# Kernel optimization log

Hardware: AMD Instinct MI355X
Metric: run time of the kernel (lower is better)

Reference implementation:

```python
import jax, jax.numpy as jnp
import numpy as np

N, E = 50000, 800000
D, H, C, ED = 128, 8, 16, 32  # in_channels, heads, head_dim, edge_dim
EPS = 1e-5

def _ln(x, g, b):
    mu = jnp.mean(x, axis=-1, keepdims=True)
    var = jnp.mean((x - mu) ** 2, axis=-1, keepdims=True)
    return (x - mu) * jax.lax.rsqrt(var + EPS) * g + b

def setup_inputs() -> dict:
    key = jax.random.key(0)
    ks = jax.random.split(key, 20)
    s = 0.05
    inp = {
        'x': jax.random.normal(ks[0], (N, D), jnp.float32),
        'edge_index': jax.random.randint(ks[1], (2, E), 0, N, jnp.int64),
        'edge_attr': jax.random.normal(ks[2], (E, ED), jnp.float32),
        'Wq': jax.random.normal(ks[3], (D, H * C)) * s,
        'bq': jnp.zeros((H * C,)),
        'Wk': jax.random.normal(ks[4], (D, H * C)) * s,
        'bk': jnp.zeros((H * C,)),
        'Wv': jax.random.normal(ks[5], (D, H * C)) * s,
        'bv': jnp.zeros((H * C,)),
        'We': jax.random.normal(ks[6], (ED, H * C)) * s,
        'Wskip': jax.random.normal(ks[7], (D, H * C)) * s,
        'bskip': jnp.zeros((H * C,)),
        'ln1_g': jnp.ones((D,)), 'ln1_b': jnp.zeros((D,)),
        'W1': jax.random.normal(ks[8], (D, 4 * D)) * s,
        'b1': jnp.zeros((4 * D,)),
        'W2': jax.random.normal(ks[9], (4 * D, D)) * s,
        'b2': jnp.zeros((D,)),
        'ln2_g': jnp.ones((D,)), 'ln2_b': jnp.zeros((D,)),
    }
    return inp

def reference(x, edge_index, edge_attr, Wq, bq, Wk, bk, Wv, bv, We, Wskip, bskip,
              ln1_g, ln1_b, W1, b1, W2, b2, ln2_g, ln2_b):
    src, dst = edge_index[0], edge_index[1]
    # node-level projections, then gather per-edge  [N,H,C] -> [E,H,C]
    q = (x @ Wq + bq).reshape(N, H, C)
    k = (x @ Wk + bk).reshape(N, H, C)
    v = (x @ Wv + bv).reshape(N, H, C)
    e = (edge_attr @ We).reshape(E, H, C)
    k_e = k[src] + e
    alpha = jnp.sum(q[dst] * k_e, axis=-1) / jnp.sqrt(jnp.float32(C))  # [E,H]
    # segment softmax over destination nodes
    m = jax.ops.segment_max(alpha, dst, num_segments=N)               # [N,H]
    p = jnp.exp(alpha - m[dst])
    denom = jax.ops.segment_sum(p, dst, num_segments=N)
    a = p / (denom[dst] + 1e-16)
    out_e = (v[src] + e) * a[..., None]                               # [E,H,C]
    attn = jax.ops.segment_sum(out_e, dst, num_segments=N).reshape(N, H * C)
    attn = attn + x @ Wskip + bskip  # root/skip connection
    # transformer block: residual + LN + FFN + LN (dropout = identity, eval)
    h = _ln(x + attn, ln1_g, ln1_b)
    ffn = jax.nn.relu(h @ W1 + b1) @ W2 + b2
    return _ln(h + ffn, ln2_g, ln2_b)
```

## Files before the change

### kernel.cpp

```cpp
#include <hip/hip_runtime.h>
#include <hip/hip_bf16.h>

using bf16 = __hip_bfloat16;
typedef __attribute__((ext_vector_type(8))) short short8;
typedef __attribute__((ext_vector_type(4))) float floatx4;

#define NN 50000
#define EE 800000
#define DD 128
#define HH 8
#define CC 16
#define EDD 32
#define DF 512

__device__ __forceinline__ float b2f(bf16 v) { return __bfloat162float(v); }
__device__ __forceinline__ float bs2f(short s) {
    bf16 h = *reinterpret_cast<bf16*>(&s);
    return __bfloat162float(h);
}
__device__ __forceinline__ float bu2f(unsigned short s) {
    unsigned int u = ((unsigned int)s) << 16;
    return *reinterpret_cast<float*>(&u);
}
__device__ __forceinline__ short f2bs(float v) {
    bf16 h = __float2bfloat16(v);
    return *reinterpret_cast<short*>(&h);
}

__global__ void k_detect(const int* __restrict__ ei, int* __restrict__ flag)
{
    if (threadIdx.x == 0 && blockIdx.x == 0) {
        int all0 = 1;
        for (int i = 0; i < 16; ++i) all0 &= (ei[2 * i + 1] == 0);
        flag[0] = all0;
    }
}

__device__ __forceinline__ int load_src(const int* ei, int is64, int i)
{
    int s = is64 ? ei[2 * i] : ei[i];
    return (s < 0) ? 0 : (s >= NN ? NN - 1 : s);
}
__device__ __forceinline__ int load_dst(const int* ei, int is64, int i)
{
    int d = is64 ? ei[2 * EE + 2 * i] : ei[EE + i];
    return (d < 0) ? 0 : (d >= NN ? NN - 1 : d);
}

__global__ void k_packall(const float* __restrict__ Wq, const float* __restrict__ Wk,
                          const float* __restrict__ Wv, const float* __restrict__ Wsk,
                          const float* __restrict__ W1, const float* __restrict__ W2,
                          const float* __restrict__ We,
                          bf16* __restrict__ wqp, bf16* __restrict__ wkp,
                          bf16* __restrict__ wvp, bf16* __restrict__ wskp,
                          bf16* __restrict__ w1p, bf16* __restrict__ w2p,
                          bf16* __restrict__ wep)
{
    int idx = blockIdx.x * 256 + threadIdx.x;
    const float* W; bf16* out; int ksteps, N, local;
    if (idx < 65536) {
        int wsel = idx >> 14; local = idx & 16383;
        W   = (wsel == 0) ? Wq  : (wsel == 1) ? Wk  : (wsel == 2) ? Wv  : Wsk;
        out = (wsel == 0) ? wqp : (wsel == 1) ? wkp : (wsel == 2) ? wvp : wskp;
        ksteps = 4; N = 128;
    } else if (idx < 131072) { local = idx - 65536;  W = W1; out = w1p; ksteps = 4;  N = 512; }
    else if (idx < 196608)   { local = idx - 131072; W = W2; out = w2p; ksteps = 16; N = 128; }
    else if (idx < 200704)   { local = idx - 196608; W = We; out = wep; ksteps = 1;  N = 128; }
    else return;
    int j = local & 7, lane = (local >> 3) & 63, rest = local >> 9;
    int kstep = rest % ksteps, ntile = rest / ksteps;
    int quad = lane >> 4, m = lane & 15;
    int k = kstep * 32 + quad * 8 + j;
    int n = ntile * 16 + m;
    out[local] = __float2bfloat16(W[(size_t)k * N + n]);
}

__global__ __launch_bounds__(256) void k_proj(
    const float* __restrict__ x,
    const bf16* __restrict__ wqp, const bf16* __restrict__ wkp,
    const bf16* __restrict__ wvp, const bf16* __restrict__ wskp,
    const float* __restrict__ bq, const float* __restrict__ bk,
    const float* __restrict__ bv, const float* __restrict__ bsk,
    bf16* __restrict__ qb, unsigned int* __restrict__ kvb,
    bf16* __restrict__ skipb)
{
    __shared__ __align__(16) short xs[32][136];
    __shared__ __align__(16) short os[32][520];
    const int t = threadIdx.x;
    const int wave = t >> 6, lane = t & 63;
    const int quad = lane >> 4, m = lane & 15;
    const int n0 = blockIdx.x * 32;

    for (int idx = t; idx < 32 * 32; idx += 256) {
        int row = idx >> 5, g = idx & 31;
        int node = n0 + row;
        float4 xv = {0.f, 0.f, 0.f, 0.f};
        if (node < NN) xv = *reinterpret_cast<const float4*>(&x[(size_t)node * 128 + g * 4]);
        short4 s4;
        s4.x = f2bs(xv.x); s4.y = f2bs(xv.y); s4.z = f2bs(xv.z); s4.w = f2bs(xv.w);
        *reinterpret_cast<short4*>(&xs[row][g * 4]) = s4;
    }
    __syncthreads();

    const bf16* Wp = (wave == 0) ? wqp : (wave == 1) ? wkp : (wave == 2) ? wvp : wskp;
    const float* bias = (wave == 0) ? bq : (wave == 1) ? bk : (wave == 2) ? bv : bsk;

    floatx4 acc[2][8];
#pragma unroll
    for (int mt = 0; mt < 2; ++mt)
#pragma unroll
        for (int nt = 0; nt < 8; ++nt) acc[mt][nt] = (floatx4){0.f, 0.f, 0.f, 0.f};

#pragma unroll
    for (int kstep = 0; kstep < 4; ++kstep) {
        short8 af0 = *reinterpret_cast<const short8*>(&xs[m][kstep * 32 + quad * 8]);
        short8 af1 = *reinterpret_cast<const short8*>(&xs[16 + m][kstep * 32 + quad * 8]);
#pragma unroll
        for (int nt = 0; nt < 8; ++nt) {
            short8 bf = *reinterpret_cast<const short8*>(
                reinterpret_cast<const short*>(Wp) + ((nt * 4 + kstep) * 64 + lane) * 8);
            acc[0][nt] = __builtin_amdgcn_mfma_f32_16x16x32_bf16(af0, bf, acc[0][nt], 0, 0, 0);
            acc[1][nt] = __builtin_amdgcn_mfma_f32_16x16x32_bf16(af1, bf, acc[1][nt], 0, 0, 0);
        }
    }
#pragma unroll
    for (int nt = 0; nt < 8; ++nt) {
        float bs = bias[nt * 16 + m];
#pragma unroll
        for (int mt = 0; mt < 2; ++mt)
#pragma unroll
            for (int r = 0; r < 4; ++r)
                os[mt * 16 + quad * 4 + r][wave * 128 + nt * 16 + m] = f2bs(acc[mt][nt][r] + bs);
    }
    __syncthreads();
    for (int idx = t; idx < 32 * 64; idx += 256) {
        int row = idx >> 6, c = idx & 63;
        int node = n0 + row;
        if (node >= NN) continue;
        unsigned int qu  = *reinterpret_cast<const unsigned int*>(&os[row][2 * c]);
        unsigned int ku  = *reinterpret_cast<const unsigned int*>(&os[row][128 + 2 * c]);
        unsigned int vu  = *reinterpret_cast<const unsigned int*>(&os[row][256 + 2 * c]);
        unsigned int sku = *reinterpret_cast<const unsigned int*>(&os[row][384 + 2 * c]);
        reinterpret_cast<unsigned int*>(qb)[(size_t)node * 64 + c] = qu;
        reinterpret_cast<unsigned int*>(skipb)[(size_t)node * 64 + c] = sku;
        uint2 kv;
        kv.x = (ku & 0xffffu) | (vu << 16);
        kv.y = (ku >> 16) | (vu & 0xffff0000u);
        reinterpret_cast<uint2*>(kvb)[(size_t)node * 64 + c] = kv;
    }
}

__global__ void k_hist(const int* __restrict__ ei, const int* __restrict__ flag,
                       int* __restrict__ deg)
{
    int i = blockIdx.x * 256 + threadIdx.x;
    if (i >= EE) return;
    atomicAdd(&deg[load_dst(ei, flag[0], i)], 1);
}

__global__ __launch_bounds__(1024) void k_scan(const int* __restrict__ deg,
                                               int* __restrict__ rowstart)
{
    __shared__ int s[1024];
    const int t = threadIdx.x;
    const int CH = 49;
    int base = t * CH;
    int sum = 0;
    for (int i = 0; i < CH; i++) {
        int idx = base + i;
        if (idx < NN) sum += deg[idx];
    }
    s[t] = sum;
    __syncthreads();
    int own = sum;
    for (int off = 1; off < 1024; off <<= 1) {
        int v = (t >= off) ? s[t - off] : 0;
        __syncthreads();
        s[t] += v;
        __syncthreads();
    }
    int run = s[t] - own;
    for (int i = 0; i < CH; i++) {
        int idx = base + i;
        if (idx < NN) {
            rowstart[idx] = run;
            run += deg[idx];
        }
    }
    if (t == 0) rowstart[NN] = EE;
}

__global__ void k_scatter(const int* __restrict__ ei, const int* __restrict__ flag,
                          const int* __restrict__ rowstart,
                          int* __restrict__ cursor, int2* __restrict__ srcid)
{
    int i = blockIdx.x * 256 + threadIdx.x;
    if (i >= EE) return;
    int is64 = flag[0];
    int d = load_dst(ei, is64, i);
    int pos = rowstart[d] + atomicAdd(&cursor[d], 1);
    srcid[pos] = make_int2(load_src(ei, is64, i), i);
}

__global__ __launch_bounds__(256) void k_attn(
    const float* __restrict__ x, const float* __restrict__ edge_attr,
    const bf16* __restrict__ wep,
    const bf16* __restrict__ qb, const unsigned int* __restrict__ kvb,
    const bf16* __restrict__ skipb,
    const int* __restrict__ rowstart, const int2* __restrict__ srcid,
    const float* __restrict__ ln1g, const float* __restrict__ ln1b,
    bf16* __restrict__ hb)
{
    __shared__ __align__(16) short es[4][16][136];
    __shared__ __align__(16) short wes[4096];
    const int t = threadIdx.x;
    const int wave = t >> 6, lane = t & 63;
    const int quad = lane >> 4, m = lane & 15;
    const int n = blockIdx.x * 4 + wave;

    for (int idx = t; idx < 512; idx += 256)
        *reinterpret_cast<short8*>(&wes[idx * 8]) =
            *reinterpret_cast<const short8*>(reinterpret_cast<const short*>(wep) + idx * 8);
    __syncthreads();

    short (*esw)[136] = es[wave];

    unsigned int qp = reinterpret_cast<const unsigned int*>(qb)[(size_t)n * 64 + lane];
    float q0 = bu2f((unsigned short)(qp & 0xffffu));
    float q1 = bu2f((unsigned short)(qp >> 16));

    const int eoff = rowstart[n], eend = rowstart[n + 1];
    float lsum = 0.f, acc0 = 0.f, acc1 = 0.f;

    for (int p0 = eoff; p0 < eend; p0 += 16) {
        int pos = p0 + m;
        int pc = (pos < eend) ? pos : eoff;
        int2 se = srcid[pc];

        const float* arow = edge_attr + (size_t)se.y * 32 + quad * 8;
        float4 a0 = *reinterpret_cast<const float4*>(arow);
        float4 a1 = *reinterpret_cast<const float4*>(arow + 4);

        uint2 kvr[16];
#pragma unroll
        for (int j = 0; j < 16; ++j) {
            int sj = __builtin_amdgcn_readlane(se.x, j);
            kvr[j] = reinterpret_cast<const uint2*>(kvb + (size_t)(unsigned)sj * 128)[lane];
        }

        short8 Af;
        Af[0] = f2bs(a0.x); Af[1] = f2bs(a0.y); Af[2] = f2bs(a0.z); Af[3] = f2bs(a0.w);
        Af[4] = f2bs(a1.x); Af[5] = f2bs(a1.y); Af[6] = f2bs(a1.z); Af[7] = f2bs(a1.w);
#pragma unroll
        for (int nt = 0; nt < 8; ++nt) {
            short8 Bf = *reinterpret_cast<const short8*>(&wes[(nt * 64 + lane) * 8]);
            floatx4 C = {0.f, 0.f, 0.f, 0.f};
            C = __builtin_amdgcn_mfma_f32_16x16x32_bf16(Af, Bf, C, 0, 0, 0);
            int col = nt * 16 + m;
#pragma unroll
            for (int r = 0; r < 4; ++r)
                esw[quad * 4 + r][col] = f2bs(C[r]);
        }
        __builtin_amdgcn_wave_barrier();

        int cnt = eend - p0; if (cnt > 16) cnt = 16;
#pragma unroll
        for (int j = 0; j < 16; ++j) {
            unsigned int eu = *reinterpret_cast<const unsigned int*>(&esw[j][2 * lane]);
            float e0 = bu2f((unsigned short)(eu & 0xffffu));
            float e1 = bu2f((unsigned short)(eu >> 16));
            float k0 = bu2f((unsigned short)(kvr[j].x & 0xffffu));
            float v0 = bu2f((unsigned short)(kvr[j].x >> 16));
            float k1 = bu2f((unsigned short)(kvr[j].y & 0xffffu));
            float v1 = bu2f((unsigned short)(kvr[j].y >> 16));
            float pr = fmaf(k1 + e1, q1, (k0 + e0) * q0);
            pr += __shfl_xor(pr, 1);
            pr += __shfl_xor(pr, 2);
            pr += __shfl_xor(pr, 4);
            float w = (j < cnt) ? __expf(pr * 0.25f) : 0.f;
            lsum += w;
            acc0 = fmaf(v0 + e0, w, acc0);
            acc1 = fmaf(v1 + e1, w, acc1);
        }
        __builtin_amdgcn_wave_barrier();
    }

    float rden = 1.f / (lsum + 1e-16f);
    float attn0 = acc0 * rden, attn1 = acc1 * rden;
    float2 xv = *reinterpret_cast<const float2*>(x + (size_t)n * 128 + 2 * lane);
    unsigned int skp = reinterpret_cast<const unsigned int*>(skipb)[(size_t)n * 64 + lane];
    float pre0 = xv.x + attn0 + bu2f((unsigned short)(skp & 0xffffu));
    float pre1 = xv.y + attn1 + bu2f((unsigned short)(skp >> 16));
    float s1 = pre0 + pre1, s2 = pre0 * pre0 + pre1 * pre1;
#pragma unroll
    for (int off = 1; off < 64; off <<= 1) {
        s1 += __shfl_xor(s1, off);
        s2 += __shfl_xor(s2, off);
    }
    float mu = s1 * (1.f / 128.f);
    float var = s2 * (1.f / 128.f) - mu * mu;
    float inv = rsqrtf(var + 1e-5f);
    float2 g  = *reinterpret_cast<const float2*>(ln1g + 2 * lane);
    float2 bb = *reinterpret_cast<const float2*>(ln1b + 2 * lane);
    float h0 = (pre0 - mu) * inv * g.x + bb.x;
    float h1 = (pre1 - mu) * inv * g.y + bb.y;
    unsigned int hu = (unsigned int)(unsigned short)f2bs(h0) |
                      ((unsigned int)(unsigned short)f2bs(h1) << 16);
    reinterpret_cast<unsigned int*>(hb)[(size_t)n * 64 + lane] = hu;
}

__global__ __launch_bounds__(256) void k_ffn(
    const bf16* __restrict__ hb,
    const bf16* __restrict__ w1p, const float* __restrict__ b1,
    const bf16* __restrict__ w2p, const float* __restrict__ b2,
    const float* __restrict__ ln2g, const float* __restrict__ ln2b,
    float* __restrict__ out)
{
    __shared__ __align__(16) short hs[32][136];
    __shared__ __align__(16) short t1s[32][520];
    float* fs = reinterpret_cast<float*>(&t1s[0][0]);
    const int t = threadIdx.x;
    const int wave = t >> 6, lane = t & 63;
    const int quad = lane >> 4, m = lane & 15;
    const int n0 = blockIdx.x * 32;

    for (int idx = t; idx < 32 * 16; idx += 256) {
        int row = idx >> 4, g = idx & 15;
        int node = n0 + row;
        if (node < NN) {
            *reinterpret_cast<float4*>(&hs[row][g * 8]) =
                *reinterpret_cast<const float4*>(&hb[(size_t)node * 128 + g * 8]);
        } else {
            float4 z = {0.f, 0.f, 0.f, 0.f};
            *reinterpret_cast<float4*>(&hs[row][g * 8]) = z;
        }
    }
    __syncthreads();

    floatx4 acc1[2][8];
#pragma unroll
    for (int mt = 0; mt < 2; ++mt)
#pragma unroll
        for (int nt = 0; nt < 8; ++nt) acc1[mt][nt] = (floatx4){0.f, 0.f, 0.f, 0.f};
#pragma unroll
    for (int kstep = 0; kstep < 4; ++kstep) {
        short8 af0 = *reinterpret_cast<const short8*>(&hs[m][kstep * 32 + quad * 8]);
        short8 af1 = *reinterpret_cast<const short8*>(&hs[16 + m][kstep * 32 + quad * 8]);
#pragma unroll
        for (int nt = 0; nt < 8; ++nt) {
            short8 bf = *reinterpret_cast<const short8*>(
                reinterpret_cast<const short*>(w1p) + (((wave * 8 + nt) * 4 + kstep) * 64 + lane) * 8);
            acc1[0][nt] = __builtin_amdgcn_mfma_f32_16x16x32_bf16(af0, bf, acc1[0][nt], 0, 0, 0);
            acc1[1][nt] = __builtin_amdgcn_mfma_f32_16x16x32_bf16(af1, bf, acc1[1][nt], 0, 0, 0);
        }
    }
#pragma unroll
    for (int nt = 0; nt < 8; ++nt) {
        float bs = b1[wave * 128 + nt * 16 + m];
#pragma unroll
        for (int mt = 0; mt < 2; ++mt)
#pragma unroll
            for (int r = 0; r < 4; ++r)
                t1s[mt * 16 + quad * 4 + r][wave * 128 + nt * 16 + m] =
                    f2bs(fmaxf(acc1[mt][nt][r] + bs, 0.f));
    }
    __syncthreads();

    floatx4 acc2[2][2];
#pragma unroll
    for (int mt = 0; mt < 2; ++mt)
#pragma unroll
        for (int nt = 0; nt < 2; ++nt) acc2[mt][nt] = (floatx4){0.f, 0.f, 0.f, 0.f};
#pragma unroll
    for (int kstep = 0; kstep < 16; ++kstep) {
        short8 af0 = *reinterpret_cast<const short8*>(&t1s[m][kstep * 32 + quad * 8]);
        short8 af1 = *reinterpret_cast<const short8*>(&t1s[16 + m][kstep * 32 + quad * 8]);
#pragma unroll
        for (int nt = 0; nt < 2; ++nt) {
            short8 bf = *reinterpret_cast<const short8*>(
                reinterpret_cast<const short*>(w2p) + (((wave * 2 + nt) * 16 + kstep) * 64 + lane) * 8);
            acc2[0][nt] = __builtin_amdgcn_mfma_f32_16x16x32_bf16(af0, bf, acc2[0][nt], 0, 0, 0);
            acc2[1][nt] = __builtin_amdgcn_mfma_f32_16x16x32_bf16(af1, bf, acc2[1][nt], 0, 0, 0);
        }
    }
    __syncthreads();
#pragma unroll
    for (int nt = 0; nt < 2; ++nt) {
        int col = (wave * 2 + nt) * 16 + m;
        float bs = b2[col];
#pragma unroll
        for (int mt = 0; mt < 2; ++mt)
#pragma unroll
            for (int r = 0; r < 4; ++r)
                fs[(mt * 16 + quad * 4 + r) * 132 + col] = acc2[mt][nt][r] + bs;
    }
    __syncthreads();

    for (int rr = 0; rr < 8; ++rr) {
        int row = wave * 8 + rr;
        int node = n0 + row;
        float p0 = bs2f(hs[row][lane]) + fs[row * 132 + lane];
        float p1 = bs2f(hs[row][lane + 64]) + fs[row * 132 + lane + 64];
        float s1 = p0 + p1, s2 = p0 * p0 + p1 * p1;
#pragma unroll
        for (int off = 1; off < 64; off <<= 1) {
            s1 += __shfl_xor(s1, off);
            s2 += __shfl_xor(s2, off);
        }
        float mu = s1 * (1.f / 128.f);
        float var = s2 * (1.f / 128.f) - mu * mu;
        float inv = rsqrtf(var + 1e-5f);
        if (node < NN) {
            out[(size_t)node * 128 + lane] = (p0 - mu) * inv * ln2g[lane] + ln2b[lane];
            out[(size_t)node * 128 + lane + 64] = (p1 - mu) * inv * ln2g[lane + 64] + ln2b[lane + 64];
        }
    }
}

extern "C" void kernel_launch(void* const* d_in, const int* in_sizes, int n_in,
                              void* d_out, int out_size, void* d_ws, size_t ws_size,
                              hipStream_t stream)
{
    const float* x    = (const float*)d_in[0];
    const int*   ei   = (const int*)d_in[1];
    const float* ea   = (const float*)d_in[2];
    const float* Wq   = (const float*)d_in[3];
    const float* bq   = (const float*)d_in[4];
    const float* Wk   = (const float*)d_in[5];
    const float* bk   = (const float*)d_in[6];
    const float* Wv   = (const float*)d_in[7];
    const float* bv   = (const float*)d_in[8];
    const float* We   = (const float*)d_in[9];
    const float* Wsk  = (const float*)d_in[10];
    const float* bsk  = (const float*)d_in[11];
    const float* ln1g = (const float*)d_in[12];
    const float* ln1b = (const float*)d_in[13];
    const float* W1   = (const float*)d_in[14];
    const float* b1   = (const float*)d_in[15];
    const float* W2   = (const float*)d_in[16];
    const float* b2   = (const float*)d_in[17];
    const float* ln2g = (const float*)d_in[18];
    const float* ln2b = (const float*)d_in[19];

    char* ws = (char*)d_ws;
    size_t off = 0;
    auto alloc = [&](size_t bytes) -> void* {
        void* p = ws + off;
        off += (bytes + 255) & ~(size_t)255;
        return p;
    };
    int*   flag     = (int*)alloc(256);
    int*   deg      = (int*)alloc((size_t)NN * 4);
    int*   cursor   = (int*)alloc((size_t)NN * 4);
    int*   rowstart = (int*)alloc((size_t)(NN + 1) * 4);
    int2*  srcid    = (int2*)alloc((size_t)EE * 8);
    bf16*  qb       = (bf16*)alloc((size_t)NN * 128 * 2);
    unsigned int* kvb = (unsigned int*)alloc((size_t)NN * 128 * 4);
    bf16*  skipb    = (bf16*)alloc((size_t)NN * 128 * 2);
    bf16*  hb       = (bf16*)alloc((size_t)NN * 128 * 2);
    bf16*  wqp      = (bf16*)alloc((size_t)16384 * 2);
    bf16*  wkp      = (bf16*)alloc((size_t)16384 * 2);
    bf16*  wvp      = (bf16*)alloc((size_t)16384 * 2);
    bf16*  wskp     = (bf16*)alloc((size_t)16384 * 2);
    bf16*  w1p      = (bf16*)alloc((size_t)65536 * 2);
    bf16*  w2p      = (bf16*)alloc((size_t)65536 * 2);
    bf16*  wep      = (bf16*)alloc((size_t)4096 * 2);

    hipMemsetAsync(deg, 0, (size_t)NN * 4, stream);
    hipMemsetAsync(cursor, 0, (size_t)NN * 4, stream);

    k_detect<<<1, 64, 0, stream>>>(ei, flag);
    k_packall<<<(200704 + 255) / 256, 256, 0, stream>>>(
        Wq, Wk, Wv, Wsk, W1, W2, We, wqp, wkp, wvp, wskp, w1p, w2p, wep);
    k_hist<<<(EE + 255) / 256, 256, 0, stream>>>(ei, flag, deg);
    k_proj<<<(NN + 31) / 32, 256, 0, stream>>>(x, wqp, wkp, wvp, wskp,
                                               bq, bk, bv, bsk, qb, kvb, skipb);
    k_scan<<<1, 1024, 0, stream>>>(deg, rowstart);
    k_scatter<<<(EE + 255) / 256, 256, 0, stream>>>(ei, flag, rowstart, cursor, srcid);
    k_attn<<<(NN + 3) / 4, 256, 0, stream>>>(x, ea, wep, qb, kvb, skipb,
                                             rowstart, srcid, ln1g, ln1b, hb);
    k_ffn<<<(NN + 31) / 32, 256, 0, stream>>>(hb, w1p, b1, w2p, b2, ln2g, ln2b, (float*)d_out);
}
```

Baseline: 548.9 us.

## Use persistent work-stealing attention kernel, transposed edge LDS, and paired-edge CSR build

The attention kernel becomes persistent: 1536 blocks pull destination nodes from a global atomic counter, which should even out load across nodes of uneven degree. The edge-feature tile in LDS is transposed so each lane reads its 16 values with a few wide loads instead of 16 separate reads. The softmax now folds 1/sqrt(C)*log2(e) into q and uses exp2 directly. The histogram and scatter kernels each handle two edges per thread with vector loads. The risks are atomic contention on the single work counter and higher register pressure from the extra LDS values held per lane.

```diff
diff --git a/kernel.cpp b/kernel.cpp
--- a/kernel.cpp
+++ b/kernel.cpp
@@ -26,6 +26,10 @@
     bf16 h = __float2bfloat16(v);
     return *reinterpret_cast<short*>(&h);
 }
+__device__ __forceinline__ unsigned short f2bu(float v) {
+    bf16 h = __float2bfloat16(v);
+    return *reinterpret_cast<unsigned short*>(&h);
+}
 
 __global__ void k_detect(const int* __restrict__ ei, int* __restrict__ flag)
 {
@@ -36,15 +40,9 @@
     }
 }
 
-__device__ __forceinline__ int load_src(const int* ei, int is64, int i)
-{
-    int s = is64 ? ei[2 * i] : ei[i];
-    return (s < 0) ? 0 : (s >= NN ? NN - 1 : s);
-}
-__device__ __forceinline__ int load_dst(const int* ei, int is64, int i)
-{
-    int d = is64 ? ei[2 * EE + 2 * i] : ei[EE + i];
-    return (d < 0) ? 0 : (d >= NN ? NN - 1 : d);
+__device__ __forceinline__ int clampn(int v)
+{
+    return (v < 0) ? 0 : (v >= NN ? NN - 1 : v);
 }
 
 __global__ void k_packall(const float* __restrict__ Wq, const float* __restrict__ Wk,
@@ -153,9 +151,19 @@
 __global__ void k_hist(const int* __restrict__ ei, const int* __restrict__ flag,
                        int* __restrict__ deg)
 {
-    int i = blockIdx.x * 256 + threadIdx.x;
-    if (i >= EE) return;
-    atomicAdd(&deg[load_dst(ei, flag[0], i)], 1);
+    int tt = blockIdx.x * 256 + threadIdx.x;
+    int i0 = tt * 2;
+    if (i0 >= EE) return;
+    int d0, d1;
+    if (flag[0]) {
+        int4 v = *reinterpret_cast<const int4*>(&ei[2 * EE + 2 * i0]);
+        d0 = v.x; d1 = v.z;
+    } else {
+        int2 v = *reinterpret_cast<const int2*>(&ei[EE + i0]);
+        d0 = v.x; d1 = v.y;
+    }
+    atomicAdd(&deg[clampn(d0)], 1);
+    atomicAdd(&deg[clampn(d1)], 1);
 }
 
 __global__ __launch_bounds__(1024) void k_scan(const int* __restrict__ deg,
@@ -194,12 +202,24 @@
                           const int* __restrict__ rowstart,
                           int* __restrict__ cursor, int2* __restrict__ srcid)
 {
-    int i = blockIdx.x * 256 + threadIdx.x;
-    if (i >= EE) return;
-    int is64 = flag[0];
-    int d = load_dst(ei, is64, i);
-    int pos = rowstart[d] + atomicAdd(&cursor[d], 1);
-    srcid[pos] = make_int2(load_src(ei, is64, i), i);
+    int tt = blockIdx.x * 256 + threadIdx.x;
+    int i0 = tt * 2;
+    if (i0 >= EE) return;
+    int d0, d1, s0, s1;
+    if (flag[0]) {
+        int4 dv = *reinterpret_cast<const int4*>(&ei[2 * EE + 2 * i0]);
+        int4 sv = *reinterpret_cast<const int4*>(&ei[2 * i0]);
+        d0 = dv.x; d1 = dv.z; s0 = sv.x; s1 = sv.z;
+    } else {
+        int2 dv = *reinterpret_cast<const int2*>(&ei[EE + i0]);
+        int2 sv = *reinterpret_cast<const int2*>(&ei[i0]);
+        d0 = dv.x; d1 = dv.y; s0 = sv.x; s1 = sv.y;
+    }
+    d0 = clampn(d0); d1 = clampn(d1);
+    int p0 = rowstart[d0] + atomicAdd(&cursor[d0], 1);
+    srcid[p0] = make_int2(clampn(s0), i0);
+    int p1 = rowstart[d1] + atomicAdd(&cursor[d1], 1);
+    srcid[p1] = make_int2(clampn(s1), i0 + 1);
 }
 
 __global__ __launch_bounds__(256) void k_attn(
@@ -209,104 +229,124 @@
     const bf16* __restrict__ skipb,
     const int* __restrict__ rowstart, const int2* __restrict__ srcid,
     const float* __restrict__ ln1g, const float* __restrict__ ln1b,
-    bf16* __restrict__ hb)
-{
-    __shared__ __align__(16) short es[4][16][136];
+    int* __restrict__ qcounter, bf16* __restrict__ hb)
+{
+    __shared__ __align__(16) short es[4][128][18];
     __shared__ __align__(16) short wes[4096];
     const int t = threadIdx.x;
     const int wave = t >> 6, lane = t & 63;
     const int quad = lane >> 4, m = lane & 15;
-    const int n = blockIdx.x * 4 + wave;
 
     for (int idx = t; idx < 512; idx += 256)
         *reinterpret_cast<short8*>(&wes[idx * 8]) =
             *reinterpret_cast<const short8*>(reinterpret_cast<const short*>(wep) + idx * 8);
     __syncthreads();
 
-    short (*esw)[136] = es[wave];
-
-    unsigned int qp = reinterpret_cast<const unsigned int*>(qb)[(size_t)n * 64 + lane];
-    float q0 = bu2f((unsigned short)(qp & 0xffffu));
-    float q1 = bu2f((unsigned short)(qp >> 16));
-
-    const int eoff = rowstart[n], eend = rowstart[n + 1];
-    float lsum = 0.f, acc0 = 0.f, acc1 = 0.f;
-
-    for (int p0 = eoff; p0 < eend; p0 += 16) {
-        int pos = p0 + m;
-        int pc = (pos < eend) ? pos : eoff;
-        int2 se = srcid[pc];
-
-        const float* arow = edge_attr + (size_t)se.y * 32 + quad * 8;
-        float4 a0 = *reinterpret_cast<const float4*>(arow);
-        float4 a1 = *reinterpret_cast<const float4*>(arow + 4);
-
-        uint2 kvr[16];
-#pragma unroll
-        for (int j = 0; j < 16; ++j) {
-            int sj = __builtin_amdgcn_readlane(se.x, j);
-            kvr[j] = reinterpret_cast<const uint2*>(kvb + (size_t)(unsigned)sj * 128)[lane];
-        }
-
-        short8 Af;
-        Af[0] = f2bs(a0.x); Af[1] = f2bs(a0.y); Af[2] = f2bs(a0.z); Af[3] = f2bs(a0.w);
-        Af[4] = f2bs(a1.x); Af[5] = f2bs(a1.y); Af[6] = f2bs(a1.z); Af[7] = f2bs(a1.w);
-#pragma unroll
-        for (int nt = 0; nt < 8; ++nt) {
-            short8 Bf = *reinterpret_cast<const short8*>(&wes[(nt * 64 + lane) * 8]);
-            floatx4 C = {0.f, 0.f, 0.f, 0.f};
-            C = __builtin_amdgcn_mfma_f32_16x16x32_bf16(Af, Bf, C, 0, 0, 0);
-            int col = nt * 16 + m;
-#pragma unroll
-            for (int r = 0; r < 4; ++r)
-                esw[quad * 4 + r][col] = f2bs(C[r]);
-        }
-        __builtin_amdgcn_wave_barrier();
-
-        int cnt = eend - p0; if (cnt > 16) cnt = 16;
-#pragma unroll
-        for (int j = 0; j < 16; ++j) {
-            unsigned int eu = *reinterpret_cast<const unsigned int*>(&esw[j][2 * lane]);
-            float e0 = bu2f((unsigned short)(eu & 0xffffu));
-            float e1 = bu2f((unsigned short)(eu >> 16));
-            float k0 = bu2f((unsigned short)(kvr[j].x & 0xffffu));
-            float v0 = bu2f((unsigned short)(kvr[j].x >> 16));
-            float k1 = bu2f((unsigned short)(kvr[j].y & 0xffffu));
-            float v1 = bu2f((unsigned short)(kvr[j].y >> 16));
-            float pr = fmaf(k1 + e1, q1, (k0 + e0) * q0);
-            pr += __shfl_xor(pr, 1);
-            pr += __shfl_xor(pr, 2);
-            pr += __shfl_xor(pr, 4);
-            float w = (j < cnt) ? __expf(pr * 0.25f) : 0.f;
-            lsum += w;
-            acc0 = fmaf(v0 + e0, w, acc0);
-            acc1 = fmaf(v1 + e1, w, acc1);
-        }
-        __builtin_amdgcn_wave_barrier();
-    }
-
-    float rden = 1.f / (lsum + 1e-16f);
-    float attn0 = acc0 * rden, attn1 = acc1 * rden;
-    float2 xv = *reinterpret_cast<const float2*>(x + (size_t)n * 128 + 2 * lane);
-    unsigned int skp = reinterpret_cast<const unsigned int*>(skipb)[(size_t)n * 64 + lane];
-    float pre0 = xv.x + attn0 + bu2f((unsigned short)(skp & 0xffffu));
-    float pre1 = xv.y + attn1 + bu2f((unsigned short)(skp >> 16));
-    float s1 = pre0 + pre1, s2 = pre0 * pre0 + pre1 * pre1;
-#pragma unroll
-    for (int off = 1; off < 64; off <<= 1) {
-        s1 += __shfl_xor(s1, off);
-        s2 += __shfl_xor(s2, off);
-    }
-    float mu = s1 * (1.f / 128.f);
-    float var = s2 * (1.f / 128.f) - mu * mu;
-    float inv = rsqrtf(var + 1e-5f);
-    float2 g  = *reinterpret_cast<const float2*>(ln1g + 2 * lane);
-    float2 bb = *reinterpret_cast<const float2*>(ln1b + 2 * lane);
-    float h0 = (pre0 - mu) * inv * g.x + bb.x;
-    float h1 = (pre1 - mu) * inv * g.y + bb.y;
-    unsigned int hu = (unsigned int)(unsigned short)f2bs(h0) |
-                      ((unsigned int)(unsigned short)f2bs(h1) << 16);
-    reinterpret_cast<unsigned int*>(hb)[(size_t)n * 64 + lane] = hu;
+    short (*esw)[18] = es[wave];
+    const float QS = 0.3606737602f;
+
+    for (;;) {
+        int n;
+        if (lane == 0) n = atomicAdd(qcounter, 1);
+        n = __builtin_amdgcn_readfirstlane(n);
+        if (n >= NN) break;
+
+        unsigned int qp = reinterpret_cast<const unsigned int*>(qb)[(size_t)n * 64 + lane];
+        float q0 = bu2f((unsigned short)(qp & 0xffffu)) * QS;
+        float q1 = bu2f((unsigned short)(qp >> 16)) * QS;
+
+        const int eoff = rowstart[n], eend = rowstart[n + 1];
+        float lsum = 0.f, acc0 = 0.f, acc1 = 0.f;
+
+        for (int p0 = eoff; p0 < eend; p0 += 16) {
+            int pos = p0 + m;
+            int pc = (pos < eend) ? pos : eoff;
+            int2 se = srcid[pc];
+
+            const float* arow = edge_attr + (size_t)se.y * 32 + quad * 8;
+            float4 a0 = *reinterpret_cast<const float4*>(arow);
+            float4 a1 = *reinterpret_cast<const float4*>(arow + 4);
+
+            uint2 kvr[16];
+#pragma unroll
+            for (int j = 0; j < 16; ++j) {
+                int sj = __builtin_amdgcn_readlane(se.x, j);
+                kvr[j] = reinterpret_cast<const uint2*>(kvb + (size_t)(unsigned)sj * 128)[lane];
+            }
+
+            short8 Af;
+            Af[0] = f2bs(a0.x); Af[1] = f2bs(a0.y); Af[2] = f2bs(a0.z); Af[3] = f2bs(a0.w);
+            Af[4] = f2bs(a1.x); Af[5] = f2bs(a1.y); Af[6] = f2bs(a1.z); Af[7] = f2bs(a1.w);
+#pragma unroll
+            for (int nt = 0; nt < 8; ++nt) {
+                short8 Bf = *reinterpret_cast<const short8*>(&wes[(nt * 64 + lane) * 8]);
+                floatx4 C = {0.f, 0.f, 0.f, 0.f};
+                C = __builtin_amdgcn_mfma_f32_16x16x32_bf16(Af, Bf, C, 0, 0, 0);
+                int col = nt * 16 + m;
+                unsigned int d0 = (unsigned int)(unsigned short)f2bs(C[0]) |
+                                  ((unsigned int)(unsigned short)f2bs(C[1]) << 16);
+                unsigned int d1 = (unsigned int)(unsigned short)f2bs(C[2]) |
+                                  ((unsigned int)(unsigned short)f2bs(C[3]) << 16);
+                unsigned int* p = reinterpret_cast<unsigned int*>(&esw[col][quad * 4]);
+                p[0] = d0; p[1] = d1;
+            }
+            __builtin_amdgcn_wave_barrier();
+
+            unsigned int ea[8], eb[8];
+            {
+                const unsigned int* ra = reinterpret_cast<const unsigned int*>(&esw[2 * lane][0]);
+                const unsigned int* rb = reinterpret_cast<const unsigned int*>(&esw[2 * lane + 1][0]);
+#pragma unroll
+                for (int jj = 0; jj < 8; ++jj) { ea[jj] = ra[jj]; eb[jj] = rb[jj]; }
+            }
+
+            int cnt = eend - p0; if (cnt > 16) cnt = 16;
+#pragma unroll
+            for (int j = 0; j < 16; ++j) {
+                unsigned int eva = ea[j >> 1], evb = eb[j >> 1];
+                float e0 = (j & 1) ? bu2f((unsigned short)(eva >> 16))
+                                   : bu2f((unsigned short)(eva & 0xffffu));
+                float e1 = (j & 1) ? bu2f((unsigned short)(evb >> 16))
+                                   : bu2f((unsigned short)(evb & 0xffffu));
+                float k0 = bu2f((unsigned short)(kvr[j].x & 0xffffu));
+                float v0 = bu2f((unsigned short)(kvr[j].x >> 16));
+                float k1 = bu2f((unsigned short)(kvr[j].y & 0xffffu));
+                float v1 = bu2f((unsigned short)(kvr[j].y >> 16));
+                float pr = fmaf(k1 + e1, q1, (k0 + e0) * q0);
+                pr += __shfl_xor(pr, 1);
+                pr += __shfl_xor(pr, 2);
+                pr += __shfl_xor(pr, 4);
+                float w = (j < cnt) ? __builtin_amdgcn_exp2f(pr) : 0.f;
+                lsum += w;
+                acc0 = fmaf(v0 + e0, w, acc0);
+                acc1 = fmaf(v1 + e1, w, acc1);
+            }
+            __builtin_amdgcn_wave_barrier();
+        }
+
+        float rden = 1.f / (lsum + 1e-16f);
+        float attn0 = acc0 * rden, attn1 = acc1 * rden;
+        float2 xv = *reinterpret_cast<const float2*>(x + (size_t)n * 128 + 2 * lane);
+        unsigned int skp = reinterpret_cast<const unsigned int*>(skipb)[(size_t)n * 64 + lane];
+        float pre0 = xv.x + attn0 + bu2f((unsigned short)(skp & 0xffffu));
+        float pre1 = xv.y + attn1 + bu2f((unsigned short)(skp >> 16));
+        float s1 = pre0 + pre1, s2 = pre0 * pre0 + pre1 * pre1;
+#pragma unroll
+        for (int off = 1; off < 64; off <<= 1) {
+            s1 += __shfl_xor(s1, off);
+            s2 += __shfl_xor(s2, off);
+        }
+        float mu = s1 * (1.f / 128.f);
+        float var = s2 * (1.f / 128.f) - mu * mu;
+        float inv = rsqrtf(var + 1e-5f);
+        float2 g  = *reinterpret_cast<const float2*>(ln1g + 2 * lane);
+        float2 bb = *reinterpret_cast<const float2*>(ln1b + 2 * lane);
+        float h0 = (pre0 - mu) * inv * g.x + bb.x;
+        float h1 = (pre1 - mu) * inv * g.y + bb.y;
+        unsigned int hu = (unsigned int)(unsigned short)f2bs(h0) |
+                          ((unsigned int)(unsigned short)f2bs(h1) << 16);
+        reinterpret_cast<unsigned int*>(hb)[(size_t)n * 64 + lane] = hu;
+    }
 }
 
 __global__ __launch_bounds__(256) void k_ffn(
@@ -450,6 +490,7 @@
         return p;
     };
     int*   flag     = (int*)alloc(256);
+    int*   qcounter = (int*)alloc(256);
     int*   deg      = (int*)alloc((size_t)NN * 4);
     int*   cursor   = (int*)alloc((size_t)NN * 4);
     int*   rowstart = (int*)alloc((size_t)(NN + 1) * 4);
@@ -468,16 +509,17 @@
 
     hipMemsetAsync(deg, 0, (size_t)NN * 4, stream);
     hipMemsetAsync(cursor, 0, (size_t)NN * 4, stream);
+    hipMemsetAsync(qcounter, 0, 4, stream);
 
     k_detect<<<1, 64, 0, stream>>>(ei, flag);
     k_packall<<<(200704 + 255) / 256, 256, 0, stream>>>(
         Wq, Wk, Wv, Wsk, W1, W2, We, wqp, wkp, wvp, wskp, w1p, w2p, wep);
-    k_hist<<<(EE + 255) / 256, 256, 0, stream>>>(ei, flag, deg);
+    k_hist<<<(EE / 2 + 255) / 256, 256, 0, stream>>>(ei, flag, deg);
     k_proj<<<(NN + 31) / 32, 256, 0, stream>>>(x, wqp, wkp, wvp, wskp,
                                                bq, bk, bv, bsk, qb, kvb, skipb);
     k_scan<<<1, 1024, 0, stream>>>(deg, rowstart);
-    k_scatter<<<(EE + 255) / 256, 256, 0, stream>>>(ei, flag, rowstart, cursor, srcid);
-    k_attn<<<(NN + 3) / 4, 256, 0, stream>>>(x, ea, wep, qb, kvb, skipb,
-                                             rowstart, srcid, ln1g, ln1b, hb);
+    k_scatter<<<(EE / 2 + 255) / 256, 256, 0, stream>>>(ei, flag, rowstart, cursor, srcid);
+    k_attn<<<1536, 256, 0, stream>>>(x, ea, wep, qb, kvb, skipb,
+                                     rowstart, srcid, ln1g, ln1b, qcounter, hb);
     k_ffn<<<(NN + 31) / 32, 256, 0, stream>>>(hb, w1p, b1, w2p, b2, ln2g, ln2b, (float*)d_out);
 }
```

Result: slower. 1.096 ms (+99.6%).
